# Optimization experiments

Hardware: AMD Instinct MI355X
Metric: run time of the kernel (lower is better)

## Reference

```python
import jax, jax.numpy as jnp
import numpy as np

B, H, W, EMB = 8, 128, 128, 6
NF = 256  # number_of_filters


def setup_inputs() -> dict:
    key = jax.random.key(0)
    ks = jax.random.split(key, 12)
    s = 0.02  # init_func-style small normal init
    image = jax.random.normal(ks[0], (B, 1, H, W), jnp.float32)
    mask_embedding = jax.random.normal(ks[1], (B, EMB, H, W), jnp.float32)
    # conv stack: 134->256 (s2), 256->512 (s2), 512->1024 (s2), 1024->1024 (s2), avgpool8, 1024->128 (1x1)
    w0 = jax.random.normal(ks[2], (NF, W + EMB, 4, 4), jnp.float32) * s
    b0 = jnp.zeros((NF,), jnp.float32)
    w1 = jax.random.normal(ks[3], (2 * NF, NF, 4, 4), jnp.float32) * s
    b1 = jnp.zeros((2 * NF,), jnp.float32)
    w2 = jax.random.normal(ks[4], (4 * NF, 2 * NF, 4, 4), jnp.float32) * s
    b2 = jnp.zeros((4 * NF,), jnp.float32)
    w3 = jax.random.normal(ks[5], (4 * NF, 4 * NF, 4, 4), jnp.float32) * s
    b3 = jnp.zeros((4 * NF,), jnp.float32)
    w4 = jax.random.normal(ks[6], (W, 4 * NF, 1, 1), jnp.float32) * s
    b4 = jnp.zeros((W,), jnp.float32)
    return dict(image=image, mask_embedding=mask_embedding,
                w0=w0, b0=b0, w1=w1, b1=b1, w2=w2, b2=b2, w3=w3, b3=b3, w4=w4, b4=b4)


def _spectral_map(image, mask_embedding):
    # Original: kspace = fft2(image); for each column i zero out all other k-space
    # columns, ifft2 (unnormalized torch.ifft => 1/(H*W)), take real part.
    # Since only column i is nonzero, ifft2 separates:
    #   sep[b,i,h,w] = Re( (1/W) * ifft_H(kspace[:, :, i])[h] * exp(2j*pi*w*i/W) )
    Bv, _, Hv, Wv = image.shape
    kspace = jnp.fft.fft2(image[:, 0])                    # (B, H, W) complex64
    col = jnp.fft.ifft(kspace, axis=1) / Wv               # (B, H, W_i); ifft over height gives 1/H
    idx = jnp.arange(Wv)
    twiddle = jnp.exp((2j * jnp.pi / Wv) * jnp.outer(idx, idx).astype(jnp.float32))  # (W_spatial, W_i) complex64
    sep = jnp.real(jnp.einsum('bhi,wi->bihw', col, twiddle))  # (B, W, H, W) float32
    return jnp.concatenate([sep, mask_embedding], axis=1)     # (B, W+EMB, H, W)


def _conv(x, w, b, stride):
    y = jax.lax.conv_general_dilated(x, w, (stride, stride), [(1, 1), (1, 1)],
                                     dimension_numbers=('NCHW', 'OIHW', 'NCHW'))
    return y + b[None, :, None, None]


def _inorm(x):  # InstanceNorm2d, affine=False, eps=1e-5
    m = jnp.mean(x, (2, 3), keepdims=True)
    v = jnp.var(x, (2, 3), keepdims=True)
    return (x - m) * jax.lax.rsqrt(v + 1e-5)


def _lrelu(x):
    return jax.nn.leaky_relu(x, 0.2)


def reference(image, mask_embedding, w0, b0, w1, b1, w2, b2, w3, b3, w4, b4):
    x = _spectral_map(image, mask_embedding)       # (B, 134, 128, 128)
    x = _lrelu(_conv(x, w0, b0, 2))                # (B, 256, 64, 64)
    x = _lrelu(_inorm(_conv(x, w1, b1, 2)))        # (B, 512, 32, 32)
    x = _lrelu(_inorm(_conv(x, w2, b2, 2)))        # (B, 1024, 16, 16)
    x = _lrelu(_inorm(_conv(x, w3, b3, 2)))        # (B, 1024, 8, 8)
    pooled = jnp.mean(x, (2, 3))                   # AvgPool(k=8) -> (B, 1024)
    out = jnp.einsum('bc,oc->bo', pooled, w4[:, :, 0, 0]) + b4  # 1x1 conv + squeeze -> (B, 128)
    return out
```

## Files before the change

kernel.cpp:

```cpp
#include <hip/hip_runtime.h>
#include <hip/hip_bf16.h>
#include <cstdint>
#include <cstddef>

typedef __attribute__((ext_vector_type(8))) short bf16x8;
typedef __attribute__((ext_vector_type(4))) float f32x4;

#define PI2F 6.283185307179586f

__device__ __forceinline__ float bf2f(unsigned short u) {
  union { float f; uint32_t i; } x; x.i = ((uint32_t)u) << 16; return x.f;
}
__device__ __forceinline__ unsigned short f2bf(float f) {
  union { float f; uint32_t i; } x; x.f = f;
  uint32_t r = x.i + 0x7FFF + ((x.i >> 16) & 1);
  return (unsigned short)(r >> 16);
}

__device__ __forceinline__ void glds16(const void* g, void* l) {
  __builtin_amdgcn_global_load_lds(
      (const __attribute__((address_space(1))) unsigned int*)g,
      (__attribute__((address_space(3))) unsigned int*)l, 16, 0, 0);
}

__global__ void zinit_kernel(unsigned short* __restrict__ zp, unsigned short* __restrict__ pad) {
  int t = threadIdx.x;
  zp[t] = 0;
  pad[t] = 0;
}

__global__ void dft_kernel(const float* __restrict__ img, float2* __restrict__ col,
                           float2* __restrict__ tw) {
  __shared__ float row[128];
  __shared__ float2 twl[128];
  const int bh = blockIdx.x;
  const int i = threadIdx.x;
  row[i] = img[bh * 128 + i];
  float s, c;
  sincosf(PI2F * (float)i / 128.0f, &s, &c);
  twl[i] = make_float2(c, s);
  __syncthreads();
  if (bh == 0) tw[i] = twl[i];
  float sr = 0.f, si = 0.f;
  for (int w = 0; w < 128; ++w) {
    float v = row[w];
    float2 t = twl[(i * w) & 127];
    sr += v * t.x;
    si -= v * t.y;
  }
  col[bh * 128 + i] = make_float2(sr * (1.0f / 128.0f), si * (1.0f / 128.0f));
}

__global__ __launch_bounds__(256)
void sep_cl_kernel(const float2* __restrict__ col, const float2* __restrict__ tw,
                   const float* __restrict__ maskE, unsigned short* __restrict__ x0) {
  __shared__ unsigned short lt[128][132];
  __shared__ float2 twl[128];
  const int bh = blockIdx.x;
  const int b = bh >> 7, h = bh & 127;
  const int tid = threadIdx.x;
  if (tid < 128) twl[tid] = tw[tid];
  __syncthreads();
  {
    const int c = tid >> 1;
    const int w0 = (tid & 1) * 64;
    float2 cv = col[(b * 128 + h) * 128 + c];
#pragma unroll 8
    for (int j = 0; j < 64; ++j) {
      int w = w0 + j;
      float2 t = twl[(w * c) & 127];
      lt[c][w] = f2bf(cv.x * t.x - cv.y * t.y);
    }
  }
  __syncthreads();
  if (tid < 144) {
    const int c = tid;
    unsigned short* dst = x0 + ((size_t)bh * 128) * 144 + c;
    if (c < 128) {
      for (int w = 0; w < 128; ++w) dst[(size_t)w * 144] = lt[c][w];
    } else if (c < 134) {
      const float* m = maskE + ((size_t)(b * 6 + (c - 128)) * 128 + h) * 128;
      for (int w = 0; w < 128; ++w) dst[(size_t)w * 144] = f2bf(m[w]);
    } else {
      for (int w = 0; w < 128; ++w) dst[(size_t)w * 144] = 0;
    }
  }
}

template<int CIN, int CINP>
__global__ __launch_bounds__(256)
void cvtperm_kernel(const float* __restrict__ src, unsigned short* __restrict__ dst) {
  __shared__ unsigned short tile[16][68];
  const int m = blockIdx.y;
  const int ci0 = blockIdx.x * 64;
  const int tid = threadIdx.x;
  {
    const int ci = ci0 + (tid >> 2);
    const int t0 = (tid & 3) * 4;
    float4 v = make_float4(0.f, 0.f, 0.f, 0.f);
    if (ci < CIN) v = *reinterpret_cast<const float4*>(&src[((size_t)m * CIN + ci) * 16 + t0]);
    const int cr = tid >> 2;
    tile[t0 + 0][cr] = f2bf(v.x);
    tile[t0 + 1][cr] = f2bf(v.y);
    tile[t0 + 2][cr] = f2bf(v.z);
    tile[t0 + 3][cr] = f2bf(v.w);
  }
  __syncthreads();
  {
    const int t = tid >> 4;
    const int co = (tid & 15) * 4;
    const int ci = ci0 + co;
    if (ci < CINP) {
      ushort4 o;
      o.x = tile[t][co]; o.y = tile[t][co + 1]; o.z = tile[t][co + 2]; o.w = tile[t][co + 3];
      *reinterpret_cast<ushort4*>(&dst[(size_t)m * (16 * CINP) + (size_t)t * CINP + ci]) = o;
    }
  }
}

template<int CINP, int CSTOR, int COUT, int HI, int WI, int HO, int WO, int NSPLIT, bool FUSED>
__global__ __launch_bounds__(256, 2)
void conv_cl4_kernel(const unsigned short* __restrict__ X,
                     const unsigned short* __restrict__ Wt,
                     const unsigned short* __restrict__ zp,
                     const float* __restrict__ bias,
                     unsigned short* __restrict__ Y,
                     float* __restrict__ P) {
  constexpr int KTOT = 16 * CINP;
  constexpr int CPT = CINP / 32;
  constexpr int HOWO = HO * WO;
  constexpr int LHW = __builtin_ctz(HOWO);
  constexpr int LWO = __builtin_ctz(WO);
  constexpr int TPS = 16 / NSPLIT;
  constexpr size_t PSTRIDE = (size_t)8 * HOWO * COUT;
  constexpr int NIT = TPS * CPT;

  __shared__ __align__(16) unsigned short As[2][4096];
  __shared__ __align__(16) unsigned short Bs[2][4096];

  const int tid = threadIdx.x;
  const int lane = tid & 63;
  const int wv = tid >> 6;
  const int wm = wv >> 1, wn = wv & 1;
  const int n0 = blockIdx.x * 128;
  const int m0 = blockIdx.y * 128;
  const int split = blockIdx.z;
  const int r = lane & 15, g = lane >> 4;

  const int row0 = tid >> 2;
  const int row1 = row0 + 64;
  const int chk = tid & 3;
  const int kofs = (((chk - ((row0 >> 1) & 3)) & 3)) * 8;

  int bb0, bho0, bwo0, bb1, bho1, bwo1;
  {
    int rn0 = n0 + row0, rn1 = n0 + row1;
    bb0 = rn0 >> LHW; bb1 = rn1 >> LHW;
    int re0 = rn0 & (HOWO - 1), re1 = rn1 & (HOWO - 1);
    bho0 = re0 >> LWO; bho1 = re1 >> LWO;
    bwo0 = re0 & (WO - 1); bwo1 = re1 & (WO - 1);
  }

  const int tap0 = split * TPS;
  int tapI = tap0, ccI = 0;
  size_t boff0, boff1; bool bok0, bok1;
  auto tap_geom = [&](int t) {
    int kh = t >> 2, kw = t & 3;
    {
      int h = 2 * bho0 - 1 + kh, w = 2 * bwo0 - 1 + kw;
      bool hv = (unsigned)h < (unsigned)HI, wvv = (unsigned)w < (unsigned)WI;
      bok0 = hv && wvv;
      boff0 = (((size_t)bb0 * HI + (hv ? h : 0)) * WI + (wvv ? w : 0)) * (size_t)CSTOR;
    }
    {
      int h = 2 * bho1 - 1 + kh, w = 2 * bwo1 - 1 + kw;
      bool hv = (unsigned)h < (unsigned)HI, wvv = (unsigned)w < (unsigned)WI;
      bok1 = hv && wvv;
      boff1 = (((size_t)bb1 * HI + (hv ? h : 0)) * WI + (wvv ? w : 0)) * (size_t)CSTOR;
    }
  };
  tap_geom(tapI);

  auto issue = [&](int buf) {
    const int kk = tapI * CINP + ccI * 32 + kofs;
    glds16(Wt + (size_t)(m0 + row0) * KTOT + kk, &As[buf][wv * 512]);
    glds16(Wt + (size_t)(m0 + row1) * KTOT + kk, &As[buf][2048 + wv * 512]);
    const int ci = ccI * 32 + kofs;
    glds16(bok0 ? (X + boff0 + ci) : zp, &Bs[buf][wv * 512]);
    glds16(bok1 ? (X + boff1 + ci) : zp, &Bs[buf][2048 + wv * 512]);
  };
  auto advance = [&]() {
    ccI++;
    if (ccI == CPT) { ccI = 0; tapI++; if (tapI < tap0 + TPS) tap_geom(tapI); }
  };

  f32x4 acc[4][4] = {};

  issue(0); advance();
  for (int it = 0; it < NIT; ++it) {
    __syncthreads();
    if (it + 1 < NIT) { issue((it + 1) & 1); advance(); }
    const int buf = it & 1;
    bf16x8 af[4], bf[4];
#pragma unroll
    for (int mi = 0; mi < 4; ++mi) {
      int rw = wm * 64 + mi * 16 + r;
      af[mi] = *reinterpret_cast<const bf16x8*>(
          &As[buf][rw * 32 + (((g + ((rw >> 1) & 3)) & 3) * 8)]);
    }
#pragma unroll
    for (int ni = 0; ni < 4; ++ni) {
      int rw = wn * 64 + ni * 16 + r;
      bf[ni] = *reinterpret_cast<const bf16x8*>(
          &Bs[buf][rw * 32 + (((g + ((rw >> 1) & 3)) & 3) * 8)]);
    }
#pragma unroll
    for (int mi = 0; mi < 4; ++mi)
#pragma unroll
      for (int ni = 0; ni < 4; ++ni)
        acc[mi][ni] = __builtin_amdgcn_mfma_f32_16x16x32_bf16(af[mi], bf[ni], acc[mi][ni], 0, 0, 0);
  }

#pragma unroll
  for (int ni = 0; ni < 4; ++ni) {
    int n = n0 + wn * 64 + ni * 16 + r;
    int b = n >> LHW;
    int rem = n & (HOWO - 1);
    size_t obase = ((size_t)b * HOWO + rem) * COUT;
#pragma unroll
    for (int mi = 0; mi < 4; ++mi) {
      int mb = m0 + wm * 64 + mi * 16 + g * 4;
      f32x4 a = acc[mi][ni];
      if constexpr (FUSED) {
        float v0 = a[0] + bias[mb + 0]; v0 = v0 > 0.f ? v0 : 0.2f * v0;
        float v1 = a[1] + bias[mb + 1]; v1 = v1 > 0.f ? v1 : 0.2f * v1;
        float v2 = a[2] + bias[mb + 2]; v2 = v2 > 0.f ? v2 : 0.2f * v2;
        float v3 = a[3] + bias[mb + 3]; v3 = v3 > 0.f ? v3 : 0.2f * v3;
        ushort4 o;
        o.x = f2bf(v0); o.y = f2bf(v1); o.z = f2bf(v2); o.w = f2bf(v3);
        *reinterpret_cast<ushort4*>(&Y[obase + mb]) = o;
      } else {
        *reinterpret_cast<float4*>(&P[split * PSTRIDE + obase + mb]) =
            make_float4(a[0], a[1], a[2], a[3]);
      }
    }
  }
}

template<int HOWO, int COUT, int NSPLIT>
__global__ __launch_bounds__(256)
void inorm_cl3_kernel(const float* __restrict__ P, unsigned short* __restrict__ Y) {
  constexpr int PER = HOWO / 32;
  constexpr size_t PSTRIDE = (size_t)8 * HOWO * COUT;
  const int b = blockIdx.y;
  const int cl = threadIdx.x & 7;
  const int c = blockIdx.x * 8 + cl;
  const int hw0 = threadIdx.x >> 3;
  const float* base = P + ((size_t)b * HOWO) * COUT + c;
  float v[PER];
  float s1 = 0.f, s2 = 0.f;
#pragma unroll
  for (int j = 0; j < PER; ++j) {
    int hw = hw0 + j * 32;
    float x = 0.f;
#pragma unroll
    for (int s = 0; s < NSPLIT; ++s) x += base[s * PSTRIDE + (size_t)hw * COUT];
    v[j] = x; s1 += x; s2 += x * x;
  }
  __shared__ float r1[32][9], r2[32][9];
  __shared__ float ms[8], rs[8];
  r1[hw0][cl] = s1; r2[hw0][cl] = s2;
  __syncthreads();
  if (threadIdx.x < 8) {
    float a1 = 0.f, a2 = 0.f;
#pragma unroll
    for (int i = 0; i < 32; ++i) { a1 += r1[i][threadIdx.x]; a2 += r2[i][threadIdx.x]; }
    float mean = a1 * (1.0f / HOWO);
    float var = a2 * (1.0f / HOWO) - mean * mean;
    ms[threadIdx.x] = mean;
    rs[threadIdx.x] = rsqrtf(var + 1e-5f);
  }
  __syncthreads();
  const float mean = ms[cl], rstd = rs[cl];
  unsigned short* yb = Y + ((size_t)b * HOWO) * COUT + c;
#pragma unroll
  for (int j = 0; j < PER; ++j) {
    int hw = hw0 + j * 32;
    float t = (v[j] - mean) * rstd;
    t = t > 0.f ? t : 0.2f * t;
    yb[(size_t)hw * COUT] = f2bf(t);
  }
}

__global__ __launch_bounds__(256)
void pool_cl_kernel(const unsigned short* __restrict__ X, float* __restrict__ pooled) {
  const int b = blockIdx.x;
  const int c4 = threadIdx.x * 4;
  float4 acc = make_float4(0.f, 0.f, 0.f, 0.f);
  for (int hw = 0; hw < 64; ++hw) {
    ushort4 v = *reinterpret_cast<const ushort4*>(&X[((size_t)b * 64 + hw) * 1024 + c4]);
    acc.x += bf2f(v.x); acc.y += bf2f(v.y); acc.z += bf2f(v.z); acc.w += bf2f(v.w);
  }
  acc.x *= (1.0f / 64.0f); acc.y *= (1.0f / 64.0f);
  acc.z *= (1.0f / 64.0f); acc.w *= (1.0f / 64.0f);
  *reinterpret_cast<float4*>(&pooled[b * 1024 + c4]) = acc;
}

__global__ __launch_bounds__(64)
void fc_kernel(const float* __restrict__ pooled, const float* __restrict__ w4,
               const float* __restrict__ b4, float* __restrict__ out) {
  const int bo = blockIdx.x;
  const int b = bo >> 7, o = bo & 127;
  const int lane = threadIdx.x;
  float s = 0.f;
#pragma unroll
  for (int j = 0; j < 16; ++j) {
    int c = lane + j * 64;
    s += pooled[b * 1024 + c] * w4[o * 1024 + c];
  }
#pragma unroll
  for (int off = 32; off > 0; off >>= 1) s += __shfl_xor(s, off);
  if (lane == 0) out[bo] = s + b4[o];
}

extern "C" void kernel_launch(void* const* d_in, const int* in_sizes, int n_in,
                              void* d_out, int out_size, void* d_ws, size_t ws_size,
                              hipStream_t stream) {
  (void)in_sizes; (void)n_in; (void)out_size; (void)ws_size;
  const float* image = (const float*)d_in[0];
  const float* maskE = (const float*)d_in[1];
  const float* w0 = (const float*)d_in[2];
  const float* b0 = (const float*)d_in[3];
  const float* w1 = (const float*)d_in[4];
  const float* w2 = (const float*)d_in[6];
  const float* w3 = (const float*)d_in[8];
  const float* w4 = (const float*)d_in[10];
  const float* b4 = (const float*)d_in[11];
  float* out = (float*)d_out;

  char* ws = (char*)d_ws;
  size_t off = 0;
  auto alloc = [&](size_t bytes) -> void* {
    void* p = ws + off;
    off = (off + bytes + 255) & ~(size_t)255;
    return p;
  };

  const size_t X0BYTES = (size_t)8 * 128 * 128 * 144 * 2;
  unsigned short* wbuf = (unsigned short*)alloc((size_t)1024 * 16384 * 2);
  char* bufA = (char*)alloc(X0BYTES + 256);
  char* bufB = (char*)alloc((size_t)8 * 4096 * 256 * 2);
  float2* col = (float2*)alloc((size_t)131072 * sizeof(float2));
  float2* tw = (float2*)alloc(128 * sizeof(float2));
  float* pooled = (float*)alloc(8192 * 4);
  unsigned short* zp = (unsigned short*)alloc(256);

  unsigned short* x0 = (unsigned short*)bufA;
  unsigned short* x0pad = (unsigned short*)(bufA + X0BYTES);
  float* part = (float*)bufA;
  unsigned short* a0 = (unsigned short*)bufB;
  unsigned short* a1 = (unsigned short*)bufB;
  unsigned short* a2 = (unsigned short*)bufB;
  unsigned short* a3 = (unsigned short*)bufB;

  zinit_kernel<<<1, 128, 0, stream>>>(zp, x0pad);

  dft_kernel<<<1024, 128, 0, stream>>>(image, col, tw);
  sep_cl_kernel<<<1024, 256, 0, stream>>>(col, tw, maskE, x0);

  cvtperm_kernel<134, 160><<<dim3(3, 256), 256, 0, stream>>>(w0, wbuf);
  conv_cl4_kernel<160, 144, 256, 128, 128, 64, 64, 1, true>
      <<<dim3(256, 2, 1), 256, 0, stream>>>(x0, wbuf, zp, b0, a0, nullptr);

  cvtperm_kernel<256, 256><<<dim3(4, 512), 256, 0, stream>>>(w1, wbuf);
  conv_cl4_kernel<256, 256, 512, 64, 64, 32, 32, 2, false>
      <<<dim3(64, 4, 2), 256, 0, stream>>>(a0, wbuf, zp, nullptr, nullptr, part);
  inorm_cl3_kernel<1024, 512, 2><<<dim3(64, 8), 256, 0, stream>>>(part, a1);

  cvtperm_kernel<512, 512><<<dim3(8, 1024), 256, 0, stream>>>(w2, wbuf);
  conv_cl4_kernel<512, 512, 1024, 32, 32, 16, 16, 4, false>
      <<<dim3(16, 8, 4), 256, 0, stream>>>(a1, wbuf, zp, nullptr, nullptr, part);
  inorm_cl3_kernel<256, 1024, 4><<<dim3(128, 8), 256, 0, stream>>>(part, a2);

  cvtperm_kernel<1024, 1024><<<dim3(16, 1024), 256, 0, stream>>>(w3, wbuf);
  conv_cl4_kernel<1024, 1024, 1024, 16, 16, 8, 8, 16, false>
      <<<dim3(4, 8, 16), 256, 0, stream>>>(a2, wbuf, zp, nullptr, nullptr, part);
  inorm_cl3_kernel<64, 1024, 16><<<dim3(128, 8), 256, 0, stream>>>(part, a3);

  pool_cl_kernel<<<8, 256, 0, stream>>>(a3, pooled);
  fc_kernel<<<1024, 64, 0, stream>>>(pooled, w4, b4, out);
}
```

Measured before the change: 334.0 us.

## Deepen conv LDS pipeline to four stages and vectorize spectral-map writes

The conv kernel goes from double to quad buffering in LDS. It issues three stages ahead and waits on explicit vmcnt counts instead of a full __syncthreads, so more global-to-LDS loads are in flight while the MFMAs run. The spectral-map kernel is rewritten so each thread produces contiguous channel vectors per pixel and writes them with ushort4 stores, replacing scattered 2-byte strided stores and dropping the LDS transpose. The LDS footprint doubles to 64KB per block, which may limit occupancy under launch_bounds(256,2). The vmcnt counts assume exactly four loads per issue.

```diff
diff --git a/kernel.cpp b/kernel.cpp
--- a/kernel.cpp
+++ b/kernel.cpp
@@ -52,38 +52,49 @@
 }
 
 __global__ __launch_bounds__(256)
-void sep_cl_kernel(const float2* __restrict__ col, const float2* __restrict__ tw,
-                   const float* __restrict__ maskE, unsigned short* __restrict__ x0) {
-  __shared__ unsigned short lt[128][132];
+void sep_cl2_kernel(const float2* __restrict__ col, const float2* __restrict__ tw,
+                    const float* __restrict__ maskE, unsigned short* __restrict__ x0) {
+  __shared__ float2 cl[128];
   __shared__ float2 twl[128];
   const int bh = blockIdx.x;
   const int b = bh >> 7, h = bh & 127;
   const int tid = threadIdx.x;
-  if (tid < 128) twl[tid] = tw[tid];
+  if (tid < 128) {
+    cl[tid] = col[(b * 128 + h) * 128 + tid];
+    twl[tid] = tw[tid];
+  }
   __syncthreads();
-  {
-    const int c = tid >> 1;
-    const int w0 = (tid & 1) * 64;
-    float2 cv = col[(b * 128 + h) * 128 + c];
-#pragma unroll 8
-    for (int j = 0; j < 64; ++j) {
-      int w = w0 + j;
-      float2 t = twl[(w * c) & 127];
-      lt[c][w] = f2bf(cv.x * t.x - cv.y * t.y);
-    }
-  }
-  __syncthreads();
-  if (tid < 144) {
-    const int c = tid;
-    unsigned short* dst = x0 + ((size_t)bh * 128) * 144 + c;
-    if (c < 128) {
-      for (int w = 0; w < 128; ++w) dst[(size_t)w * 144] = lt[c][w];
-    } else if (c < 134) {
-      const float* m = maskE + ((size_t)(b * 6 + (c - 128)) * 128 + h) * 128;
-      for (int w = 0; w < 128; ++w) dst[(size_t)w * 144] = f2bf(m[w]);
-    } else {
-      for (int w = 0; w < 128; ++w) dst[(size_t)w * 144] = 0;
-    }
+  const int p = tid >> 1;
+  const int c0 = (tid & 1) * 64;
+  unsigned short* dst = x0 + ((size_t)bh * 128 + p) * 144;
+#pragma unroll
+  for (int j = 0; j < 16; ++j) {
+    ushort4 o;
+#pragma unroll
+    for (int q = 0; q < 4; ++q) {
+      int c = c0 + 4 * j + q;
+      float2 cv = cl[c];
+      float2 t = twl[(p * c) & 127];
+      float v = cv.x * t.x - cv.y * t.y;
+      ((unsigned short*)&o)[q] = f2bf(v);
+    }
+    *reinterpret_cast<ushort4*>(dst + c0 + 4 * j) = o;
+  }
+  if (tid < 128) {
+    const int w = tid;
+    float v[6];
+#pragma unroll
+    for (int cm = 0; cm < 6; ++cm)
+      v[cm] = maskE[(((size_t)(b * 6 + cm) * 128) + h) * 128 + w];
+    unsigned short* d2 = x0 + ((size_t)bh * 128 + w) * 144 + 128;
+    ushort4 m0, m1, mz;
+    m0.x = f2bf(v[0]); m0.y = f2bf(v[1]); m0.z = f2bf(v[2]); m0.w = f2bf(v[3]);
+    m1.x = f2bf(v[4]); m1.y = f2bf(v[5]); m1.z = 0; m1.w = 0;
+    mz.x = 0; mz.y = 0; mz.z = 0; mz.w = 0;
+    reinterpret_cast<ushort4*>(d2)[0] = m0;
+    reinterpret_cast<ushort4*>(d2)[1] = m1;
+    reinterpret_cast<ushort4*>(d2)[2] = mz;
+    reinterpret_cast<ushort4*>(d2)[3] = mz;
   }
 }
 
@@ -120,7 +131,7 @@
 
 template<int CINP, int CSTOR, int COUT, int HI, int WI, int HO, int WO, int NSPLIT, bool FUSED>
 __global__ __launch_bounds__(256, 2)
-void conv_cl4_kernel(const unsigned short* __restrict__ X,
+void conv_cl5_kernel(const unsigned short* __restrict__ X,
                      const unsigned short* __restrict__ Wt,
                      const unsigned short* __restrict__ zp,
                      const float* __restrict__ bias,
@@ -135,8 +146,8 @@
   constexpr size_t PSTRIDE = (size_t)8 * HOWO * COUT;
   constexpr int NIT = TPS * CPT;
 
-  __shared__ __align__(16) unsigned short As[2][4096];
-  __shared__ __align__(16) unsigned short Bs[2][4096];
+  __shared__ __align__(16) unsigned short As[4][4096];
+  __shared__ __align__(16) unsigned short Bs[4][4096];
 
   const int tid = threadIdx.x;
   const int lane = tid & 63;
@@ -197,10 +208,17 @@
   f32x4 acc[4][4] = {};
 
   issue(0); advance();
+  issue(1); advance();
+  issue(2); advance();
+
   for (int it = 0; it < NIT; ++it) {
-    __syncthreads();
-    if (it + 1 < NIT) { issue((it + 1) & 1); advance(); }
-    const int buf = it & 1;
+    if (it + 2 < NIT)      asm volatile("s_waitcnt vmcnt(8)" ::: "memory");
+    else if (it + 1 < NIT) asm volatile("s_waitcnt vmcnt(4)" ::: "memory");
+    else                   asm volatile("s_waitcnt vmcnt(0)" ::: "memory");
+    __builtin_amdgcn_s_barrier();
+    __builtin_amdgcn_sched_barrier(0);
+    if (it + 3 < NIT) { issue((it + 3) & 3); advance(); }
+    const int buf = it & 3;
     bf16x8 af[4], bf[4];
 #pragma unroll
     for (int mi = 0; mi < 4; ++mi) {
@@ -366,24 +384,24 @@
   zinit_kernel<<<1, 128, 0, stream>>>(zp, x0pad);
 
   dft_kernel<<<1024, 128, 0, stream>>>(image, col, tw);
-  sep_cl_kernel<<<1024, 256, 0, stream>>>(col, tw, maskE, x0);
+  sep_cl2_kernel<<<1024, 256, 0, stream>>>(col, tw, maskE, x0);
 
   cvtperm_kernel<134, 160><<<dim3(3, 256), 256, 0, stream>>>(w0, wbuf);
-  conv_cl4_kernel<160, 144, 256, 128, 128, 64, 64, 1, true>
+  conv_cl5_kernel<160, 144, 256, 128, 128, 64, 64, 1, true>
       <<<dim3(256, 2, 1), 256, 0, stream>>>(x0, wbuf, zp, b0, a0, nullptr);
 
   cvtperm_kernel<256, 256><<<dim3(4, 512), 256, 0, stream>>>(w1, wbuf);
-  conv_cl4_kernel<256, 256, 512, 64, 64, 32, 32, 2, false>
+  conv_cl5_kernel<256, 256, 512, 64, 64, 32, 32, 2, false>
       <<<dim3(64, 4, 2), 256, 0, stream>>>(a0, wbuf, zp, nullptr, nullptr, part);
   inorm_cl3_kernel<1024, 512, 2><<<dim3(64, 8), 256, 0, stream>>>(part, a1);
 
   cvtperm_kernel<512, 512><<<dim3(8, 1024), 256, 0, stream>>>(w2, wbuf);
-  conv_cl4_kernel<512, 512, 1024, 32, 32, 16, 16, 4, false>
+  conv_cl5_kernel<512, 512, 1024, 32, 32, 16, 16, 4, false>
       <<<dim3(16, 8, 4), 256, 0, stream>>>(a1, wbuf, zp, nullptr, nullptr, part);
   inorm_cl3_kernel<256, 1024, 4><<<dim3(128, 8), 256, 0, stream>>>(part, a2);
 
   cvtperm_kernel<1024, 1024><<<dim3(16, 1024), 256, 0, stream>>>(w3, wbuf);
-  conv_cl4_kernel<1024, 1024, 1024, 16, 16, 8, 8, 16, false>
+  conv_cl5_kernel<1024, 1024, 1024, 16, 16, 8, 8, 16, false>
       <<<dim3(4, 8, 16), 256, 0, stream>>>(a2, wbuf, zp, nullptr, nullptr, part);
   inorm_cl3_kernel<64, 1024, 16><<<dim3(128, 8), 256, 0, stream>>>(part, a3);
 
```

New measurement: 338.0 us. No clear change (+1.2%).
